# Kernel tuning notes

Measured on AMD Instinct MI355X. Metric: run time of the kernel, lower is better.

Reference implementation:

```python
import jax, jax.numpy as jnp
import numpy as np

B, H, W, EMB = 8, 32, 32, 768
N_HEADS, HEAD = 12, 64
RATIO = 4
EPS = 1e-5


def layer_norm(x, g, b):
    m = jnp.mean(x, axis=-1, keepdims=True)
    v = jnp.var(x, axis=-1, keepdims=True)
    return (x - m) * jax.lax.rsqrt(v + EPS) * g + b


def block(x, g, b, W1, b1, W2, b2):
    # Block(in, out, ratio): LayerNorm -> Linear(in, in*ratio) -> GELU -> Linear(in*ratio, out)
    y = layer_norm(x, g, b)
    y = jax.nn.gelu(y @ W1 + b1, approximate=False)
    return y @ W2 + b2


def _mk_block_params(key, d_in, d_out, ratio=RATIO):
    hid = int(d_in * ratio)
    k1, k2 = jax.random.split(key)
    return (
        jnp.ones((d_in,), jnp.float32),            # ln gamma
        jnp.zeros((d_in,), jnp.float32),           # ln beta
        jax.random.normal(k1, (d_in, hid), jnp.float32) * 0.02,
        jnp.zeros((hid,), jnp.float32),
        jax.random.normal(k2, (hid, d_out), jnp.float32) * 0.02,
        jnp.zeros((d_out,), jnp.float32),
    )


def setup_inputs() -> dict:
    key = jax.random.key(0)
    kx, kq, kp, km = jax.random.split(key, 4)
    x = jax.random.normal(kx, (B, H, W, EMB), jnp.float32)
    qkv = _mk_block_params(kq, EMB, 3 * N_HEADS * HEAD)
    proj = _mk_block_params(kp, N_HEADS * HEAD, EMB)
    mlp = _mk_block_params(km, EMB, EMB)
    names = ["g", "b", "W1", "b1", "W2", "b2"]
    out = {"x": x}
    for pre, p in (("qkv", qkv), ("proj", proj), ("mlp", mlp)):
        for n, v in zip(names, p):
            out[f"{pre}_{n}"] = v
    return out


def reference(x, qkv_g, qkv_b, qkv_W1, qkv_b1, qkv_W2, qkv_b2,
              proj_g, proj_b, proj_W1, proj_b1, proj_W2, proj_b2,
              mlp_g, mlp_b, mlp_W1, mlp_b1, mlp_W2, mlp_b2):
    b, h, w, c = x.shape
    seq = h * w
    scale = 1.0 / HEAD ** 0.5

    t = block(x, qkv_g, qkv_b, qkv_W1, qkv_b1, qkv_W2, qkv_b2)  # (b,h,w,3*n*s)
    # Rearrange 'b h w (k n s) -> k (b n) (h w) s'
    t = t.reshape(b, seq, 3, N_HEADS, HEAD).transpose(2, 0, 3, 1, 4)
    t = t.reshape(3, b * N_HEADS, seq, HEAD)
    q, k, v = t[0], t[1], t[2]

    score = jnp.einsum('btc,blc->btl', q, k)          # (b*n, seq, seq)
    attn = jax.nn.softmax(score * scale, axis=2)
    out = jnp.einsum('btc,btl->blc', v, attn)          # (b*n, seq, head) -- attn^T @ v, as in source

    # Rearrange '(b n) (h w) s -> b h w (n s)'
    out = out.reshape(b, N_HEADS, h, w, HEAD).transpose(0, 2, 3, 1, 4)
    out = out.reshape(b, h, w, N_HEADS * HEAD)

    y = block(out, proj_g, proj_b, proj_W1, proj_b1, proj_W2, proj_b2)
    y = block(y, mlp_g, mlp_b, mlp_W1, mlp_b1, mlp_W2, mlp_b2)
    return y
```

## Files before the change

### kernel.cpp

```cpp
#include <hip/hip_runtime.h>
#include <stdint.h>


typedef unsigned short u16;
typedef __attribute__((ext_vector_type(8))) short bf16x8;
typedef __attribute__((ext_vector_type(4))) float f32x4;
typedef __attribute__((address_space(1))) unsigned int as1_u32;
typedef __attribute__((address_space(3))) unsigned int as3_u32;

__device__ __forceinline__ float bf2f(u16 u) {
  union { unsigned int i; float f; } v; v.i = ((unsigned int)u) << 16; return v.f;
}
__device__ __forceinline__ u16 f2bf(float f) {
  union { float f; unsigned int i; } v; v.f = f;
  unsigned int r = v.i + 0x7fffu + ((v.i >> 16) & 1u);
  return (u16)(r >> 16);
}
__device__ __forceinline__ float gelu_exact(float x) {
  return 0.5f * x * (1.0f + erff(x * 0.70710678118654752f));
}
__device__ __forceinline__ void async_ld16(const u16* g, u16* l) {
  __builtin_amdgcn_global_load_lds((const as1_u32*)g, (as3_u32*)l, 16, 0, 0);
}

__global__ __launch_bounds__(256) void ln_kernel(const void* __restrict__ xv,
                                                 const float* __restrict__ g,
                                                 const float* __restrict__ be,
                                                 u16* __restrict__ out, int inF32) {
  int token = blockIdx.x, tid = threadIdx.x;
  int wave = tid >> 6, lane = tid & 63;
  float v0, v1, v2;
  if (inF32) {
    const float* row = (const float*)xv + (size_t)token * 768;
    v0 = row[tid]; v1 = row[tid + 256]; v2 = row[tid + 512];
  } else {
    const u16* row = (const u16*)xv + (size_t)token * 768;
    v0 = bf2f(row[tid]); v1 = bf2f(row[tid + 256]); v2 = bf2f(row[tid + 512]);
  }
  float s = v0 + v1 + v2;
  float q = v0 * v0 + v1 * v1 + v2 * v2;
#pragma unroll
  for (int m = 1; m < 64; m <<= 1) { s += __shfl_xor(s, m); q += __shfl_xor(q, m); }
  __shared__ float red[8];
  if (lane == 0) { red[wave] = s; red[4 + wave] = q; }
  __syncthreads();
  s = red[0] + red[1] + red[2] + red[3];
  q = red[4] + red[5] + red[6] + red[7];
  float mean = s * (1.0f / 768.0f);
  float var  = q * (1.0f / 768.0f) - mean * mean;
  float inv  = rsqrtf(var + 1e-5f);
  u16* o = out + (size_t)token * 768;
  o[tid]       = f2bf((v0 - mean) * inv * g[tid]       + be[tid]);
  o[tid + 256] = f2bf((v1 - mean) * inv * g[tid + 256] + be[tid + 256]);
  o[tid + 512] = f2bf((v2 - mean) * inv * g[tid + 512] + be[tid + 512]);
}

__global__ __launch_bounds__(256) void transpose_f32_bf16(const float* __restrict__ in,
                                                          u16* __restrict__ out,
                                                          int R, int Cc) {
  __shared__ u16 tile[32][33];
  int c0 = blockIdx.x * 32, r0 = blockIdx.y * 32;
  int tx = threadIdx.x, ty = threadIdx.y;
  for (int i = ty; i < 32; i += 8)
    tile[i][tx] = f2bf(in[(size_t)(r0 + i) * Cc + c0 + tx]);
  __syncthreads();
  for (int i = ty; i < 32; i += 8)
    out[(size_t)(c0 + i) * R + r0 + tx] = tile[tx][i];
}

__global__ __launch_bounds__(256) void vtrans(const u16* __restrict__ t,
                                              u16* __restrict__ vt) {
  int bh = blockIdx.z, b = bh / 12, h = bh % 12;
  int t0 = blockIdx.x * 32, c0 = blockIdx.y * 32;
  __shared__ u16 tile[32][33];
  int tx = threadIdx.x, ty = threadIdx.y;
  for (int i = ty; i < 32; i += 8)
    tile[i][tx] = t[(size_t)(b * 1024 + t0 + i) * 2304 + 1536 + h * 64 + c0 + tx];
  __syncthreads();
  for (int i = ty; i < 32; i += 8)
    vt[(size_t)bh * 65536 + (size_t)(c0 + i) * 1024 + t0 + tx] = tile[tx][i];
}

#define BM 128
#define BN 128
#define BKK 64

__global__ __launch_bounds__(256, 4) void gemm_mfma(
    const u16* __restrict__ A, int lda,
    const u16* __restrict__ B, int ldb,
    void* __restrict__ C, int ldc,
    int M, int N, int K,
    const float* __restrict__ bias, int act, int cF32) {
  __shared__ u16 As[BM * BKK];
  __shared__ u16 Bs[BN * BKK];
  int m0 = blockIdx.y * BM, n0 = blockIdx.x * BN;
  int tid = threadIdx.x;
  int wave = tid >> 6, lane = tid & 63;
  int quad = lane >> 4, lo = lane & 15;
  int wr = (wave >> 1) * 64, wc = (wave & 1) * 64;

  f32x4 acc[4][4];
#pragma unroll
  for (int i = 0; i < 4; ++i)
#pragma unroll
    for (int j = 0; j < 4; ++j) acc[i][j] = (f32x4){0.f, 0.f, 0.f, 0.f};

  for (int k0 = 0; k0 < K; k0 += BKK) {
#pragma unroll
    for (int p = 0; p < 4; ++p) {
      int idx = tid + p * 256;
      int row = idx >> 3;
      int gch = ((idx & 7) ^ (row & 7)) * 8;
      int ldsOff = (wave * 64 + p * 256) * 8;
      async_ld16(A + (long long)(m0 + row) * lda + k0 + gch, As + ldsOff);
      async_ld16(B + (long long)(n0 + row) * ldb + k0 + gch, Bs + ldsOff);
    }
    __syncthreads();
#pragma unroll
    for (int ks = 0; ks < 2; ++ks) {
      bf16x8 af[4], bf[4];
#pragma unroll
      for (int i = 0; i < 4; ++i) {
        int m = wr + i * 16 + lo;
        int slot = (ks * 4 + quad) ^ (m & 7);
        af[i] = *(const bf16x8*)(As + m * BKK + slot * 8);
      }
#pragma unroll
      for (int j = 0; j < 4; ++j) {
        int n = wc + j * 16 + lo;
        int slot = (ks * 4 + quad) ^ (n & 7);
        bf[j] = *(const bf16x8*)(Bs + n * BKK + slot * 8);
      }
#pragma unroll
      for (int i = 0; i < 4; ++i)
#pragma unroll
        for (int j = 0; j < 4; ++j)
          acc[i][j] = __builtin_amdgcn_mfma_f32_16x16x32_bf16(af[i], bf[j], acc[i][j], 0, 0, 0);
    }
    __syncthreads();
  }

#pragma unroll
  for (int j = 0; j < 4; ++j) {
    int col = n0 + wc + j * 16 + lo;
    float bv = bias ? bias[col] : 0.0f;
#pragma unroll
    for (int i = 0; i < 4; ++i) {
      int rb = m0 + wr + i * 16 + quad * 4;
#pragma unroll
      for (int r = 0; r < 4; ++r) {
        int row = rb + r;
        float v = acc[i][j][r] + bv;
        if (act) v = gelu_exact(v);
        long long ci = (long long)row * ldc + col;
        if (cF32) ((float*)C)[ci] = v;
        else      ((u16*)C)[ci] = f2bf(v);
      }
    }
  }
}

__global__ __launch_bounds__(256, 2) void zstats(const u16* __restrict__ tb,
                                                 float* __restrict__ zinv) {
  int bh = blockIdx.y, b = bh / 12, h = bh % 12;
  int t0 = blockIdx.x * 128;
  __shared__ u16 Qs[128 * 64];
  __shared__ u16 Ks[128 * 64];
  __shared__ float zred[4][128];
  int tid = threadIdx.x, wave = tid >> 6, lane = tid & 63;
  int quad = lane >> 4, lo = lane & 15;
  const u16* qbase = tb + (size_t)(b * 1024) * 2304 + h * 64;
  const u16* kbase = qbase + 768;

#pragma unroll
  for (int p = 0; p < 4; ++p) {
    int idx = tid + p * 256, row = idx >> 3;
    int ch = ((idx & 7) ^ (row & 7)) * 8;
    async_ld16(qbase + (size_t)(t0 + row) * 2304 + ch, Qs + (wave * 64 + p * 256) * 8);
  }
  float zacc[8];
#pragma unroll
  for (int j = 0; j < 8; ++j) zacc[j] = 0.f;

  for (int lt = 0; lt < 8; ++lt) {
#pragma unroll
    for (int p = 0; p < 4; ++p) {
      int idx = tid + p * 256, row = idx >> 3;
      int ch = ((idx & 7) ^ (row & 7)) * 8;
      async_ld16(kbase + (size_t)(lt * 128 + row) * 2304 + ch, Ks + (wave * 64 + p * 256) * 8);
    }
    __syncthreads();
    f32x4 acc[2][8];
#pragma unroll
    for (int i = 0; i < 2; ++i)
#pragma unroll
      for (int j = 0; j < 8; ++j) acc[i][j] = (f32x4){0.f, 0.f, 0.f, 0.f};
#pragma unroll
    for (int ks = 0; ks < 2; ++ks) {
      bf16x8 af[2], bf[8];
#pragma unroll
      for (int i = 0; i < 2; ++i) {
        int m = wave * 32 + i * 16 + lo;
        int slot = (ks * 4 + quad) ^ (m & 7);
        af[i] = *(const bf16x8*)(Ks + m * 64 + slot * 8);
      }
#pragma unroll
      for (int j = 0; j < 8; ++j) {
        int n = j * 16 + lo;
        int slot = (ks * 4 + quad) ^ (n & 7);
        bf[j] = *(const bf16x8*)(Qs + n * 64 + slot * 8);
      }
#pragma unroll
      for (int i = 0; i < 2; ++i)
#pragma unroll
        for (int j = 0; j < 8; ++j)
          acc[i][j] = __builtin_amdgcn_mfma_f32_16x16x32_bf16(af[i], bf[j], acc[i][j], 0, 0, 0);
    }
#pragma unroll
    for (int j = 0; j < 8; ++j)
#pragma unroll
      for (int i = 0; i < 2; ++i)
#pragma unroll
        for (int r = 0; r < 4; ++r)
          zacc[j] += __expf(acc[i][j][r] * 0.125f);
    __syncthreads();
  }
#pragma unroll
  for (int j = 0; j < 8; ++j) {
    float v = zacc[j];
    v += __shfl_xor(v, 16);
    v += __shfl_xor(v, 32);
    zacc[j] = v;
  }
  if (quad == 0)
#pragma unroll
    for (int j = 0; j < 8; ++j) zred[wave][j * 16 + lo] = zacc[j];
  __syncthreads();
  if (tid < 128) {
    float z = zred[0][tid] + zred[1][tid] + zred[2][tid] + zred[3][tid];
    zinv[(size_t)bh * 1024 + t0 + tid] = 1.0f / z;
  }
}

__global__ __launch_bounds__(256, 2) void attn_out(const u16* __restrict__ tb,
                                                   const u16* __restrict__ vt,
                                                   const float* __restrict__ zinv,
                                                   u16* __restrict__ ao) {
  int bh = blockIdx.y, b = bh / 12, h = bh % 12;
  int l0 = blockIdx.x * 128;
  __shared__ u16 Ks[128 * 64];
  __shared__ u16 Qs[64 * 64];
  __shared__ u16 Vs[64 * 64];
  __shared__ u16 Es[128 * 64];
  int tid = threadIdx.x, wave = tid >> 6, lane = tid & 63;
  int quad = lane >> 4, lo = lane & 15;
  const u16* qbase = tb + (size_t)(b * 1024) * 2304 + h * 64;
  const u16* kbase = qbase + 768;
  const u16* vbase = vt + (size_t)bh * 65536;
  const float* zf = zinv + (size_t)bh * 1024;

#pragma unroll
  for (int p = 0; p < 4; ++p) {
    int idx = tid + p * 256, row = idx >> 3;
    int ch = ((idx & 7) ^ (row & 7)) * 8;
    async_ld16(kbase + (size_t)(l0 + row) * 2304 + ch, Ks + (wave * 64 + p * 256) * 8);
  }
  f32x4 oacc[2][4];
#pragma unroll
  for (int i = 0; i < 2; ++i)
#pragma unroll
    for (int j = 0; j < 4; ++j) oacc[i][j] = (f32x4){0.f, 0.f, 0.f, 0.f};

  for (int tt = 0; tt < 16; ++tt) {
    int t0 = tt * 64;
#pragma unroll
    for (int p = 0; p < 2; ++p) {
      int idx = tid + p * 256, row = idx >> 3;
      int ch = ((idx & 7) ^ (row & 7)) * 8;
      async_ld16(qbase + (size_t)(t0 + row) * 2304 + ch, Qs + (wave * 64 + p * 256) * 8);
      async_ld16(vbase + (size_t)row * 1024 + t0 + ch, Vs + (wave * 64 + p * 256) * 8);
    }
    __syncthreads();
    f32x4 sacc[2][4];
#pragma unroll
    for (int i = 0; i < 2; ++i)
#pragma unroll
      for (int j = 0; j < 4; ++j) sacc[i][j] = (f32x4){0.f, 0.f, 0.f, 0.f};
#pragma unroll
    for (int ks = 0; ks < 2; ++ks) {
      bf16x8 af[2], bq[4];
#pragma unroll
      for (int i = 0; i < 2; ++i) {
        int m = wave * 32 + i * 16 + lo;
        int slot = (ks * 4 + quad) ^ (m & 7);
        af[i] = *(const bf16x8*)(Ks + m * 64 + slot * 8);
      }
#pragma unroll
      for (int j = 0; j < 4; ++j) {
        int n = j * 16 + lo;
        int slot = (ks * 4 + quad) ^ (n & 7);
        bq[j] = *(const bf16x8*)(Qs + n * 64 + slot * 8);
      }
#pragma unroll
      for (int i = 0; i < 2; ++i)
#pragma unroll
        for (int j = 0; j < 4; ++j)
          sacc[i][j] = __builtin_amdgcn_mfma_f32_16x16x32_bf16(af[i], bq[j], sacc[i][j], 0, 0, 0);
    }
#pragma unroll
    for (int j = 0; j < 4; ++j) {
      int t_loc = j * 16 + lo;
      float zi = zf[t0 + t_loc];
      int ch = t_loc >> 3, pos = t_loc & 7;
#pragma unroll
      for (int i = 0; i < 2; ++i)
#pragma unroll
        for (int r = 0; r < 4; ++r) {
          int l_loc = wave * 32 + i * 16 + quad * 4 + r;
          float e = __expf(sacc[i][j][r] * 0.125f) * zi;
          Es[l_loc * 64 + ((ch ^ (l_loc & 7)) * 8 + pos)] = f2bf(e);
        }
    }
#pragma unroll
    for (int ks = 0; ks < 2; ++ks) {
      bf16x8 ae[2], bv[4];
#pragma unroll
      for (int i = 0; i < 2; ++i) {
        int m = wave * 32 + i * 16 + lo;
        int slot = (ks * 4 + quad) ^ (m & 7);
        ae[i] = *(const bf16x8*)(Es + m * 64 + slot * 8);
      }
#pragma unroll
      for (int j = 0; j < 4; ++j) {
        int n = j * 16 + lo;
        int slot = (ks * 4 + quad) ^ (n & 7);
        bv[j] = *(const bf16x8*)(Vs + n * 64 + slot * 8);
      }
#pragma unroll
      for (int i = 0; i < 2; ++i)
#pragma unroll
        for (int j = 0; j < 4; ++j)
          oacc[i][j] = __builtin_amdgcn_mfma_f32_16x16x32_bf16(ae[i], bv[j], oacc[i][j], 0, 0, 0);
    }
    __syncthreads();
  }
#pragma unroll
  for (int j = 0; j < 4; ++j) {
    int c = j * 16 + lo;
#pragma unroll
    for (int i = 0; i < 2; ++i)
#pragma unroll
      for (int r = 0; r < 4; ++r) {
        int l = l0 + wave * 32 + i * 16 + quad * 4 + r;
        ao[(size_t)(b * 1024 + l) * 768 + h * 64 + c] = f2bf(oacc[i][j][r]);
      }
  }
}

static void run_block(hipStream_t stream, const void* inp, int inF32,
                      const float* g, const float* be,
                      const float* W1, const float* b1, const float* W2, const float* b2,
                      int N2, void* outp, int outF32,
                      u16* xn, u16* hS, u16* wt1, u16* wt2) {
  transpose_f32_bf16<<<dim3(3072 / 32, 768 / 32), dim3(32, 8), 0, stream>>>(W1, wt1, 768, 3072);
  transpose_f32_bf16<<<dim3(N2 / 32, 3072 / 32), dim3(32, 8), 0, stream>>>(W2, wt2, 3072, N2);
  ln_kernel<<<8192, 256, 0, stream>>>(inp, g, be, xn, inF32);
  gemm_mfma<<<dim3(3072 / 128, 8192 / 128), dim3(256), 0, stream>>>(
      xn, 768, wt1, 768, hS, 3072, 8192, 3072, 768, b1, 1, 0);
  gemm_mfma<<<dim3(N2 / 128, 8192 / 128), dim3(256), 0, stream>>>(
      hS, 3072, wt2, 3072, outp, N2, 8192, N2, 3072, b2, 0, outF32);
}

extern "C" void kernel_launch(void* const* d_in, const int* in_sizes, int n_in,
                              void* d_out, int out_size, void* d_ws, size_t ws_size,
                              hipStream_t stream) {
  const float* x       = (const float*)d_in[0];
  const float* qkv_g   = (const float*)d_in[1];
  const float* qkv_b   = (const float*)d_in[2];
  const float* qkv_W1  = (const float*)d_in[3];
  const float* qkv_b1  = (const float*)d_in[4];
  const float* qkv_W2  = (const float*)d_in[5];
  const float* qkv_b2  = (const float*)d_in[6];
  const float* proj_g  = (const float*)d_in[7];
  const float* proj_b  = (const float*)d_in[8];
  const float* proj_W1 = (const float*)d_in[9];
  const float* proj_b1 = (const float*)d_in[10];
  const float* proj_W2 = (const float*)d_in[11];
  const float* proj_b2 = (const float*)d_in[12];
  const float* mlp_g   = (const float*)d_in[13];
  const float* mlp_b   = (const float*)d_in[14];
  const float* mlp_W1  = (const float*)d_in[15];
  const float* mlp_b1  = (const float*)d_in[16];
  const float* mlp_W2  = (const float*)d_in[17];
  const float* mlp_b2  = (const float*)d_in[18];

  u16* ws  = (u16*)d_ws;
  u16* xn  = ws;
  u16* tb  = ws + 6291456;
  u16* ao  = ws + 25165824;
  u16* yb  = ws + 31457280;
  u16* vt  = ws + 37748736;
  u16* wt1 = ws + 44040192;
  u16* wt2 = ws + 46399488;
  u16* hS  = ws + 53477376;
  float* zinv = (float*)xn;

  run_block(stream, x, 1, qkv_g, qkv_b, qkv_W1, qkv_b1, qkv_W2, qkv_b2, 2304,
            tb, 0, xn, hS, wt1, wt2);

  vtrans<<<dim3(32, 2, 96), dim3(32, 8), 0, stream>>>(tb, vt);
  zstats<<<dim3(8, 96), dim3(256), 0, stream>>>(tb, zinv);
  attn_out<<<dim3(8, 96), dim3(256), 0, stream>>>(tb, vt, zinv, ao);

  run_block(stream, ao, 0, proj_g, proj_b, proj_W1, proj_b1, proj_W2, proj_b2, 768,
            yb, 0, xn, hS, wt1, wt2);
  run_block(stream, yb, 0, mlp_g, mlp_b, mlp_W1, mlp_b1, mlp_W2, mlp_b2, 768,
            d_out, 1, xn, hS, wt1, wt2);
}
```

Before: 733.1 us.

## Split-K the narrow 768-wide GEMMs and remap tiles across XCDs

The two N=768 second-layer GEMMs (proj and mlp) now run as split-K with two partial fp32 outputs. Their sum is folded into the next LayerNorm's input load or into a final add kernel. The goal is to double the block count for these GEMMs, which otherwise launch only 384 blocks. The GEMM also remaps block indices so that consecutive row tiles land on the same XCD, improving L2 reuse. The cost is extra fp32 partial-result traffic and one added elementwise kernel.

```diff
diff --git a/kernel.cpp b/kernel.cpp
--- a/kernel.cpp
+++ b/kernel.cpp
@@ -8,6 +8,8 @@
 typedef __attribute__((address_space(1))) unsigned int as1_u32;
 typedef __attribute__((address_space(3))) unsigned int as3_u32;
 
+#define PHALF 6291456
+
 __device__ __forceinline__ float bf2f(u16 u) {
   union { unsigned int i; float f; } v; v.i = ((unsigned int)u) << 16; return v.f;
 }
@@ -26,13 +28,19 @@
 __global__ __launch_bounds__(256) void ln_kernel(const void* __restrict__ xv,
                                                  const float* __restrict__ g,
                                                  const float* __restrict__ be,
-                                                 u16* __restrict__ out, int inF32) {
+                                                 u16* __restrict__ out, int inMode) {
   int token = blockIdx.x, tid = threadIdx.x;
   int wave = tid >> 6, lane = tid & 63;
   float v0, v1, v2;
-  if (inF32) {
+  if (inMode == 1) {
     const float* row = (const float*)xv + (size_t)token * 768;
     v0 = row[tid]; v1 = row[tid + 256]; v2 = row[tid + 512];
+  } else if (inMode == 2) {
+    const float* row = (const float*)xv + (size_t)token * 768;
+    const float* row2 = row + PHALF;
+    v0 = row[tid] + row2[tid];
+    v1 = row[tid + 256] + row2[tid + 256];
+    v2 = row[tid + 512] + row2[tid + 512];
   } else {
     const u16* row = (const u16*)xv + (size_t)token * 768;
     v0 = bf2f(row[tid]); v1 = bf2f(row[tid + 256]); v2 = bf2f(row[tid + 512]);
@@ -81,6 +89,14 @@
     vt[(size_t)bh * 65536 + (size_t)(c0 + i) * 1024 + t0 + tx] = tile[tx][i];
 }
 
+__global__ __launch_bounds__(256) void add2_kernel(const float* __restrict__ P,
+                                                   float* __restrict__ out) {
+  int idx = blockIdx.x * 256 + threadIdx.x;
+  const f32x4* p0 = (const f32x4*)P;
+  const f32x4* p1 = (const f32x4*)(P + PHALF);
+  ((f32x4*)out)[idx] = p0[idx] + p1[idx];
+}
+
 #define BM 128
 #define BN 128
 #define BKK 64
@@ -89,11 +105,21 @@
     const u16* __restrict__ A, int lda,
     const u16* __restrict__ B, int ldb,
     void* __restrict__ C, int ldc,
-    int M, int N, int K,
-    const float* __restrict__ bias, int act, int cF32) {
+    int M, int N, int kSplit,
+    const float* __restrict__ bias, int act, int cF32, long long cZStride) {
   __shared__ u16 As[BM * BKK];
   __shared__ u16 Bs[BN * BKK];
-  int m0 = blockIdx.y * BM, n0 = blockIdx.x * BN;
+  int gx = gridDim.x, gy = gridDim.y;
+  int bx, by;
+  if ((gy & 7) == 0) {
+    int lin = blockIdx.y * gx + blockIdx.x;
+    int xcd = lin & 7, s = lin >> 3;
+    int r = s / gx;
+    by = xcd * (gy >> 3) + r;
+    bx = s - r * gx;
+  } else { bx = blockIdx.x; by = blockIdx.y; }
+  int m0 = by * BM, n0 = bx * BN;
+  int kOff = blockIdx.z * kSplit;
   int tid = threadIdx.x;
   int wave = tid >> 6, lane = tid & 63;
   int quad = lane >> 4, lo = lane & 15;
@@ -105,7 +131,7 @@
 #pragma unroll
     for (int j = 0; j < 4; ++j) acc[i][j] = (f32x4){0.f, 0.f, 0.f, 0.f};
 
-  for (int k0 = 0; k0 < K; k0 += BKK) {
+  for (int k0 = kOff; k0 < kOff + kSplit; k0 += BKK) {
 #pragma unroll
     for (int p = 0; p < 4; ++p) {
       int idx = tid + p * 256;
@@ -140,10 +166,11 @@
     __syncthreads();
   }
 
+  long long cZ = (long long)blockIdx.z * cZStride;
 #pragma unroll
   for (int j = 0; j < 4; ++j) {
     int col = n0 + wc + j * 16 + lo;
-    float bv = bias ? bias[col] : 0.0f;
+    float bv = (bias && blockIdx.z == 0) ? bias[col] : 0.0f;
 #pragma unroll
     for (int i = 0; i < 4; ++i) {
       int rb = m0 + wr + i * 16 + quad * 4;
@@ -152,7 +179,7 @@
         int row = rb + r;
         float v = acc[i][j][r] + bv;
         if (act) v = gelu_exact(v);
-        long long ci = (long long)row * ldc + col;
+        long long ci = cZ + (long long)row * ldc + col;
         if (cF32) ((float*)C)[ci] = v;
         else      ((u16*)C)[ci] = f2bf(v);
       }
@@ -355,20 +382,6 @@
         ao[(size_t)(b * 1024 + l) * 768 + h * 64 + c] = f2bf(oacc[i][j][r]);
       }
   }
-}
-
-static void run_block(hipStream_t stream, const void* inp, int inF32,
-                      const float* g, const float* be,
-                      const float* W1, const float* b1, const float* W2, const float* b2,
-                      int N2, void* outp, int outF32,
-                      u16* xn, u16* hS, u16* wt1, u16* wt2) {
-  transpose_f32_bf16<<<dim3(3072 / 32, 768 / 32), dim3(32, 8), 0, stream>>>(W1, wt1, 768, 3072);
-  transpose_f32_bf16<<<dim3(N2 / 32, 3072 / 32), dim3(32, 8), 0, stream>>>(W2, wt2, 3072, N2);
-  ln_kernel<<<8192, 256, 0, stream>>>(inp, g, be, xn, inF32);
-  gemm_mfma<<<dim3(3072 / 128, 8192 / 128), dim3(256), 0, stream>>>(
-      xn, 768, wt1, 768, hS, 3072, 8192, 3072, 768, b1, 1, 0);
-  gemm_mfma<<<dim3(N2 / 128, 8192 / 128), dim3(256), 0, stream>>>(
-      hS, 3072, wt2, 3072, outp, N2, 8192, N2, 3072, b2, 0, outF32);
 }
 
 extern "C" void kernel_launch(void* const* d_in, const int* in_sizes, int n_in,
@@ -404,16 +417,34 @@
   u16* wt2 = ws + 46399488;
   u16* hS  = ws + 53477376;
   float* zinv = (float*)xn;
-
-  run_block(stream, x, 1, qkv_g, qkv_b, qkv_W1, qkv_b1, qkv_W2, qkv_b2, 2304,
-            tb, 0, xn, hS, wt1, wt2);
+  float* Pf  = (float*)tb;
+
+  transpose_f32_bf16<<<dim3(96, 24), dim3(32, 8), 0, stream>>>(qkv_W1, wt1, 768, 3072);
+  transpose_f32_bf16<<<dim3(72, 96), dim3(32, 8), 0, stream>>>(qkv_W2, wt2, 3072, 2304);
+  ln_kernel<<<8192, 256, 0, stream>>>(x, qkv_g, qkv_b, xn, 1);
+  gemm_mfma<<<dim3(24, 64), dim3(256), 0, stream>>>(
+      xn, 768, wt1, 768, hS, 3072, 8192, 3072, 768, qkv_b1, 1, 0, 0);
+  gemm_mfma<<<dim3(18, 64), dim3(256), 0, stream>>>(
+      hS, 3072, wt2, 3072, tb, 2304, 8192, 2304, 3072, qkv_b2, 0, 0, 0);
 
   vtrans<<<dim3(32, 2, 96), dim3(32, 8), 0, stream>>>(tb, vt);
   zstats<<<dim3(8, 96), dim3(256), 0, stream>>>(tb, zinv);
   attn_out<<<dim3(8, 96), dim3(256), 0, stream>>>(tb, vt, zinv, ao);
 
-  run_block(stream, ao, 0, proj_g, proj_b, proj_W1, proj_b1, proj_W2, proj_b2, 768,
-            yb, 0, xn, hS, wt1, wt2);
-  run_block(stream, yb, 0, mlp_g, mlp_b, mlp_W1, mlp_b1, mlp_W2, mlp_b2, 768,
-            d_out, 1, xn, hS, wt1, wt2);
-}
+  transpose_f32_bf16<<<dim3(96, 24), dim3(32, 8), 0, stream>>>(proj_W1, wt1, 768, 3072);
+  transpose_f32_bf16<<<dim3(24, 96), dim3(32, 8), 0, stream>>>(proj_W2, wt2, 3072, 768);
+  ln_kernel<<<8192, 256, 0, stream>>>(ao, proj_g, proj_b, xn, 0);
+  gemm_mfma<<<dim3(24, 64), dim3(256), 0, stream>>>(
+      xn, 768, wt1, 768, hS, 3072, 8192, 3072, 768, proj_b1, 1, 0, 0);
+  gemm_mfma<<<dim3(6, 64, 2), dim3(256), 0, stream>>>(
+      hS, 3072, wt2, 3072, Pf, 768, 8192, 768, 1536, proj_b2, 0, 1, PHALF);
+
+  transpose_f32_bf16<<<dim3(96, 24), dim3(32, 8), 0, stream>>>(mlp_W1, wt1, 768, 3072);
+  transpose_f32_bf16<<<dim3(24, 96), dim3(32, 8), 0, stream>>>(mlp_W2, wt2, 3072, 768);
+  ln_kernel<<<8192, 256, 0, stream>>>(Pf, mlp_g, mlp_b, xn, 2);
+  gemm_mfma<<<dim3(24, 64), dim3(256), 0, stream>>>(
+      xn, 768, wt1, 768, hS, 3072, 8192, 3072, 768, mlp_b1, 1, 0, 0);
+  gemm_mfma<<<dim3(6, 64, 2), dim3(256), 0, stream>>>(
+      hS, 3072, wt2, 3072, Pf, 768, 8192, 768, 1536, mlp_b2, 0, 1, PHALF);
+  add2_kernel<<<6144, 256, 0, stream>>>(Pf, (float*)d_out);
+}
```

Result: faster. 706.6 us (-3.6%).
